# Optimization experiments

Measured on AMD Instinct MI355X. Metric: run time of the kernel, lower is better.

Reference implementation:

```python
import jax, jax.numpy as jnp
import numpy as np

IN_F, HID, OUT_F = 171, 1024, 171

def _cond_lst(condition_num, groundtruth_num, seq_len):
    num_cycles = seq_len // (condition_num + groundtruth_num) + 1
    lst = np.zeros((num_cycles, condition_num + groundtruth_num), dtype=np.float32)
    lst[:, :groundtruth_num] = 1.0
    return lst.reshape(-1)[:seq_len]

def setup_inputs() -> dict:
    key = jax.random.key(0)
    ks = jax.random.split(key, 16)
    s = 0.02
    inp = {
        'real_seq': jax.random.normal(ks[0], (128, 128, IN_F), jnp.float32),
        'W_ih1': jax.random.normal(ks[1], (4 * HID, IN_F), jnp.float32) * s,
        'W_hh1': jax.random.normal(ks[2], (4 * HID, HID), jnp.float32) * s,
        'b_ih1': jnp.zeros((4 * HID,), jnp.float32),
        'b_hh1': jnp.zeros((4 * HID,), jnp.float32),
        'W_ih2': jax.random.normal(ks[3], (4 * HID, HID), jnp.float32) * s,
        'W_hh2': jax.random.normal(ks[4], (4 * HID, HID), jnp.float32) * s,
        'b_ih2': jnp.zeros((4 * HID,), jnp.float32),
        'b_hh2': jnp.zeros((4 * HID,), jnp.float32),
        'W_ih3': jax.random.normal(ks[5], (4 * HID, HID), jnp.float32) * s,
        'W_hh3': jax.random.normal(ks[6], (4 * HID, HID), jnp.float32) * s,
        'b_ih3': jnp.zeros((4 * HID,), jnp.float32),
        'b_hh3': jnp.zeros((4 * HID,), jnp.float32),
        'W_dec': jax.random.normal(ks[7], (OUT_F, HID), jnp.float32) * s,
        'b_dec': jnp.zeros((OUT_F,), jnp.float32),
        'condition_num': 5,
        'groundtruth_num': 5,
    }
    return inp

def _lstm_cell(x, h, c, Wih, Whh, bih, bhh):
    # PyTorch LSTMCell: gates ordered i, f, g, o
    g = x @ Wih.T + bih + h @ Whh.T + bhh
    i, f, gg, o = jnp.split(g, 4, axis=-1)
    c2 = jax.nn.sigmoid(f) * c + jax.nn.sigmoid(i) * jnp.tanh(gg)
    h2 = jax.nn.sigmoid(o) * jnp.tanh(c2)
    return h2, c2

def reference(real_seq, W_ih1, W_hh1, b_ih1, b_hh1, W_ih2, W_hh2, b_ih2, b_hh2,
              W_ih3, W_hh3, b_ih3, b_hh3, W_dec, b_dec, condition_num, groundtruth_num):
    B, T, _ = real_seq.shape
    cond = jnp.asarray(_cond_lst(condition_num, groundtruth_num, T))  # [T], 1=use ground truth
    z = jnp.zeros((B, HID), jnp.float32)
    carry0 = (z, z, z, z, z, z, jnp.zeros((B, OUT_F), jnp.float32))
    xs = (jnp.swapaxes(real_seq, 0, 1), cond)  # time-major

    def step(carry, x):
        h0, h1, h2, c0, c1, c2, out_frame = carry
        frame, c_flag = x
        in_frame = jnp.where(c_flag > 0.5, frame, out_frame)
        h0, c0 = _lstm_cell(in_frame, h0, c0, W_ih1, W_hh1, b_ih1, b_hh1)
        h1, c1 = _lstm_cell(h0, h1, c1, W_ih2, W_hh2, b_ih2, b_hh2)
        h2, c2 = _lstm_cell(h1, h2, c2, W_ih3, W_hh3, b_ih3, b_hh3)
        out_frame = h2 @ W_dec.T + b_dec
        return (h0, h1, h2, c0, c1, c2, out_frame), out_frame

    _, out_seq = jax.lax.scan(step, carry0, xs)  # [T, B, OUT_F]
    return jnp.swapaxes(out_seq, 0, 1)  # [B, T, OUT_F]
```

## Files before the change

kernel.cpp:

```cpp
#include <hip/hip_runtime.h>

#define TT 128
#define INF 171

typedef _Float16 half8 __attribute__((ext_vector_type(8)));
typedef float floatx4 __attribute__((ext_vector_type(4)));
typedef unsigned short u16;

#define XBSZ 163840
#define HSZ  131072

__device__ __forceinline__ u16 f2h(float f){
  _Float16 h = (_Float16)f;
  return __builtin_bit_cast(u16, h);
}
__device__ __forceinline__ float sigm(float x){ return 1.f/(1.f+__expf(-x)); }
__device__ __forceinline__ float tanh_(float x){ return 1.f - 2.f/(__expf(2.f*x)+1.f); }

__device__ __forceinline__ void scat_coh(u16* buf, int nch, int b, int k, u16 v){
  u16* p = buf + (size_t)((((b>>4)*nch + (k>>5))*4 + ((k>>3)&3))*16 + (b&15))*8 + (k&7);
  unsigned int vv = v;
  asm volatile("global_store_short %0, %1, off sc0 sc1" :: "v"(p), "v"(vv) : "memory");
}
__device__ __forceinline__ void ld16_coh(half8& d, const u16* p){
  asm volatile("global_load_dwordx4 %0, %1, off sc0 sc1" : "=&v"(d) : "v"(p) : "memory");
}

__global__ __launch_bounds__(256) void prep_w1f(const float* __restrict__ Wih1,
    const float* __restrict__ Whh1, u16* __restrict__ Wf){
  int u = blockIdx.x*256 + threadIdx.x;
  int tile = u / 2560;
  int r = u - tile*2560;
  int kc = r >> 6, l = r & 63;
  int row = (tile>>6)*1024 + (tile&63)*16 + (l&15);
  int k0 = kc*32 + ((l>>4)<<3);
  half8 hv;
  #pragma unroll
  for (int e=0;e<8;e++){
    int k = k0+e;
    float w = 0.f;
    if (k < 171)       w = Wih1[(size_t)row*171 + k];
    else if (k < 1195) w = Whh1[(size_t)row*1024 + (k-171)];
    hv[e] = (_Float16)w;
  }
  *(half8*)&Wf[(size_t)(tile*40 + kc)*512 + (size_t)l*8] = hv;
}

__global__ __launch_bounds__(256) void prep_w23f(const float* __restrict__ Wih2,
    const float* __restrict__ Whh2, const float* __restrict__ Wih3,
    const float* __restrict__ Whh3, u16* __restrict__ W2f, u16* __restrict__ W3f){
  int u = blockIdx.x*256 + threadIdx.x;
  int tile = u >> 12;
  int r = u & 4095;
  int kc = r >> 6, l = r & 63;
  int row = (tile>>6)*1024 + (tile&63)*16 + (l&15);
  int k0 = kc*32 + ((l>>4)<<3);
  half8 h2, h3;
  #pragma unroll
  for (int e=0;e<8;e++){
    int k = k0+e;
    size_t si = (size_t)row*1024 + (k & 1023);
    h2[e] = (_Float16)((k < 1024) ? Wih2[si] : Whh2[si]);
    h3[e] = (_Float16)((k < 1024) ? Wih3[si] : Whh3[si]);
  }
  size_t base = (size_t)(tile*64 + kc)*512 + (size_t)l*8;
  *(half8*)&W2f[base] = h2;
  *(half8*)&W3f[base] = h3;
}

__global__ __launch_bounds__(256) void prep_wdecf(const float* __restrict__ Wdec,
    u16* __restrict__ Wdf){
  int u = blockIdx.x*256 + threadIdx.x;
  int tile = u / 2048;
  int r = u & 2047;
  int kc = r >> 6, l = r & 63;
  int row = tile*16 + (l&15);
  int k0 = kc*32 + ((l>>4)<<3);
  half8 hv;
  #pragma unroll
  for (int e=0;e<8;e++){
    int k = k0+e;
    hv[e] = (_Float16)((row < 171) ? Wdec[(size_t)row*1024 + k] : 0.f);
  }
  *(half8*)&Wdf[(size_t)(tile*32 + kc)*512 + (size_t)l*8] = hv;
}

__global__ __launch_bounds__(256) void prep_misc(
    const float* __restrict__ rseq, const int* __restrict__ gnp,
    const float* __restrict__ bih1, const float* __restrict__ bhh1,
    const float* __restrict__ bih2, const float* __restrict__ bhh2,
    const float* __restrict__ bih3, const float* __restrict__ bhh3,
    const float* __restrict__ bdec,
    u16* __restrict__ Xb1f, u16* __restrict__ Hf, float* __restrict__ cbuf,
    float* __restrict__ b1, float* __restrict__ b2, float* __restrict__ b3,
    float* __restrict__ bd, int* __restrict__ bar)
{
  size_t idx = (size_t)blockIdx.x*256 + threadIdx.x;
  if (idx < 327680){
    int q = (int)(idx / 163840);
    int rem = (int)(idx % 163840);
    int btile = rem / 20480;
    int r2 = rem % 20480;
    int kc = r2 >> 9, r3 = r2 & 511;
    int l = r3 >> 3, e = r3 & 7;
    int b = btile*16 + (l&15);
    int k = kc*32 + ((l>>4)<<3) + e;
    float v = 0.f;
    if (q==0 && k < 171 && *gnp > 0) v = rseq[(size_t)b*TT*INF + k];
    Xb1f[idx] = f2h(v);
    return;
  }
  idx -= 327680;
  if (idx < 786432){ Hf[idx] = 0; return; }
  idx -= 786432;
  if (idx < 393216){ cbuf[idx] = 0.f; return; }
  idx -= 393216;
  if (idx < 12288){
    int which = (int)(idx >> 12), j = (int)(idx & 4095);
    float v = (which==0)? (bih1[j]+bhh1[j]) : (which==1)? (bih2[j]+bhh2[j]) : (bih3[j]+bhh3[j]);
    ((which==0)?b1:(which==1)?b2:b3)[j] = v;
    return;
  }
  idx -= 12288;
  if (idx < 176){ bd[idx] = (idx < 171) ? bdec[idx] : 0.f; return; }
  idx -= 176;
  if (idx < 512) bar[idx] = 0;
}

__device__ __forceinline__ void gridbar(int* __restrict__ bar, int bId, int bc, int* s_dead){
  asm volatile("s_waitcnt vmcnt(0)" ::: "memory");
  __syncthreads();
  if (threadIdx.x == 0 && !(*s_dead)){
    int* c1  = &bar[(bId & 7) * 32];
    int* c0  = &bar[288];
    int* gen = &bar[320];
    bool released = false;
    int o1 = __hip_atomic_fetch_add(c1, 1, __ATOMIC_RELAXED, __HIP_MEMORY_SCOPE_AGENT);
    if ((o1 & 31) == 31){
      int o0 = __hip_atomic_fetch_add(c0, 1, __ATOMIC_RELAXED, __HIP_MEMORY_SCOPE_AGENT);
      if ((o0 & 7) == 7){
        __hip_atomic_fetch_add(gen, 1, __ATOMIC_RELAXED, __HIP_MEMORY_SCOPE_AGENT);
        released = true;
      }
    }
    if (!released){
      long long t0 = clock64();
      while (__hip_atomic_fetch_add(gen, 0, __ATOMIC_RELAXED, __HIP_MEMORY_SCOPE_AGENT) < bc + 1){
        __builtin_amdgcn_s_sleep(8);
        if (clock64() - t0 > 30000000LL){ *s_dead = 1; break; }
      }
    }
  }
  __syncthreads();
}

template<int NC, int NBC>
__device__ __forceinline__ void stage(const u16* const* srcs, u16* XL, int tid){
  half8 v[NC*NBC];
  #pragma unroll
  for (int c=0;c<NC;c++){
    #pragma unroll
    for (int i=0;i<NBC;i++)
      ld16_coh(v[c*NBC+i], srcs[c] + (size_t)i*4096 + (size_t)tid*8);
  }
  asm volatile("s_waitcnt vmcnt(0)" ::: "memory");
  __builtin_amdgcn_sched_barrier(0);
  #pragma unroll
  for (int c=0;c<NC;c++){
    #pragma unroll
    for (int i=0;i<NBC;i++)
      *(half8*)&XL[(size_t)(c*NBC+i)*4096 + (size_t)tid*8] = v[c*NBC+i];
  }
}

template<int KHALF, int GS, bool NT>
__device__ __forceinline__ void gemm_lds(const u16* __restrict__ wp,
    const u16* __restrict__ x0, const u16* __restrict__ x1,
    floatx4& a0, floatx4& a1)
{
  constexpr int NG = KHALF/GS;
  half8 W[2][GS];
  #pragma unroll
  for (int i=0;i<GS;i++)
    W[0][i] = NT ? __builtin_nontemporal_load((const half8*)(wp + (size_t)i*512))
                 : *(const half8*)(wp + (size_t)i*512);
  #pragma unroll
  for (int g8=0; g8<NG; g8++){
    const int cur = g8 & 1, nxt = cur ^ 1;
    if (g8+1 < NG){
      const size_t off = (size_t)(g8+1)*GS*512;
      #pragma unroll
      for (int i=0;i<GS;i++)
        W[nxt][i] = NT ? __builtin_nontemporal_load((const half8*)(wp + off + (size_t)i*512))
                       : *(const half8*)(wp + off + (size_t)i*512);
    }
    #pragma unroll
    for (int i=0;i<GS;i++){
      half8 xv0 = *(const half8*)(x0 + (size_t)(g8*GS+i)*512);
      half8 xv1 = *(const half8*)(x1 + (size_t)(g8*GS+i)*512);
      a0 = __builtin_amdgcn_mfma_f32_16x16x32_f16(W[cur][i], xv0, a0, 0,0,0);
      a1 = __builtin_amdgcn_mfma_f32_16x16x32_f16(W[cur][i], xv1, a1, 0,0,0);
    }
  }
}

template<bool NT>
__device__ __forceinline__ void layer23(
    const u16* __restrict__ Wl, const float* __restrict__ bb, float* __restrict__ cb,
    const u16* __restrict__ xa, const u16* __restrict__ xh, u16* __restrict__ hd,
    u16* XL, float (*gb)[16][33],
    int js, int nq, int tid, int w, int l, int g, int hf, int l15, int lq)
{
  const u16* srcs[4] = {
    xa + (size_t)(nq*2  )*16384, xa + (size_t)(nq*2+1)*16384,
    xh + (size_t)(nq*2  )*16384, xh + (size_t)(nq*2+1)*16384 };
  stage<4,4>(srcs, XL, tid);
  __syncthreads();
  const u16* wp = Wl + ((size_t)(g*64 + js)*64 + (size_t)hf*32)*512 + (size_t)(l<<3);
  const u16* x0 = XL + (size_t)hf*32768 + (size_t)(l<<3);
  const u16* x1 = x0 + 16384;
  floatx4 a0{}, a1{};
  gemm_lds<32,8,NT>(wp, x0, x1, a0, a1);
  #pragma unroll
  for (int r=0;r<4;r++){
    gb[w][lq*4+r][l15]      = a0[r];
    gb[w][lq*4+r][16 + l15] = a1[r];
  }
  __syncthreads();
  {
    int uu = tid >> 5, bq = tid & 31;
    int j = js*16 + uu, bg = nq*32 + bq;
    float gi = gb[0][uu][bq] + gb[1][uu][bq] + bb[j];
    float gf = gb[2][uu][bq] + gb[3][uu][bq] + bb[1024 + j];
    float gg = gb[4][uu][bq] + gb[5][uu][bq] + bb[2048 + j];
    float go = gb[6][uu][bq] + gb[7][uu][bq] + bb[3072 + j];
    size_t ci = (size_t)j*128 + bg;
    float c = sigm(gf)*cb[ci] + sigm(gi)*tanh_(gg);
    cb[ci] = c;
    u16 hb = f2h(sigm(go)*tanh_(c));
    scat_coh(hd, 32, bg, j, hb);
  }
}

__global__ void __launch_bounds__(512,2) acro_persist(
    const u16* __restrict__ W1f, const u16* __restrict__ W2f,
    const u16* __restrict__ W3f, const u16* __restrict__ Wdf,
    u16* __restrict__ Xb1f, u16* __restrict__ Hf, float* __restrict__ cbuf,
    const float* __restrict__ b1, const float* __restrict__ b2,
    const float* __restrict__ b3, const float* __restrict__ bd,
    const float* __restrict__ rseq, float* __restrict__ out,
    const int* __restrict__ cnp, const int* __restrict__ gnp, int* __restrict__ bar)
{
  __shared__ u16 XL[65536];
  __shared__ float gb[8][16][33];
  __shared__ int s_dead;
  const int bId = (int)blockIdx.x;
  const int js = (bId & 7)*8 + ((bId >> 5) & 7);
  const int nq = (bId >> 3) & 3;
  const int tid = (int)threadIdx.x;
  const int w = tid >> 6, l = tid & 63;
  const int g = w >> 1, hf = w & 1;
  const int l15 = l & 15, lq = l >> 4;
  if (tid == 0) s_dead = 0;
  const int gnv = *gnp;
  int P = *cnp + gnv; if (P < 1) P = 1;
  int bc = 0;

  u16* H0[2] = { Hf,          Hf + HSZ   };
  u16* H1[2] = { Hf + 2*HSZ,  Hf + 3*HSZ };
  u16* H2[2] = { Hf + 4*HSZ,  Hf + 5*HSZ };

  __syncthreads();
  for (int t=0; t<TT; t++){
    const int pr = t & 1, nx = pr ^ 1;

    {
      const u16* xb = Xb1f + (size_t)pr*XBSZ;
      const u16* srcs[2] = { xb + (size_t)(nq*2)*20480, xb + (size_t)(nq*2+1)*20480 };
      stage<2,5>(srcs, XL, tid);
      __syncthreads();
      const u16* wp = W1f + ((size_t)(g*64 + js)*40 + (size_t)hf*20)*512 + (size_t)(l<<3);
      const u16* x0 = XL + (size_t)hf*10240 + (size_t)(l<<3);
      const u16* x1 = x0 + 20480;
      floatx4 a0{}, a1{};
      gemm_lds<20,4,false>(wp, x0, x1, a0, a1);
      #pragma unroll
      for (int r=0;r<4;r++){
        gb[w][lq*4+r][l15]      = a0[r];
        gb[w][lq*4+r][16 + l15] = a1[r];
      }
      __syncthreads();
      {
        int uu = tid >> 5, bq = tid & 31;
        int j = js*16 + uu, bg = nq*32 + bq;
        float gi = gb[0][uu][bq] + gb[1][uu][bq] + b1[j];
        float gf = gb[2][uu][bq] + gb[3][uu][bq] + b1[1024 + j];
        float gg = gb[4][uu][bq] + gb[5][uu][bq] + b1[2048 + j];
        float go = gb[6][uu][bq] + gb[7][uu][bq] + b1[3072 + j];
        size_t ci = (size_t)j*128 + bg;
        float c = sigm(gf)*cbuf[ci] + sigm(gi)*tanh_(gg);
        cbuf[ci] = c;
        u16 hb = f2h(sigm(go)*tanh_(c));
        scat_coh(H0[pr], 32, bg, j, hb);
        scat_coh(Xb1f + (size_t)nx*XBSZ, 40, bg, 171 + j, hb);
      }
    }
    gridbar(bar, bId, bc, &s_dead); bc++;

    layer23<false>(W2f, b2, cbuf + 131072, H0[pr], H1[nx], H1[pr],
                   XL, gb, js, nq, tid, w, l, g, hf, l15, lq);
    gridbar(bar, bId, bc, &s_dead); bc++;
    layer23<true >(W3f, b3, cbuf + 262144, H1[pr], H2[nx], H2[pr],
                   XL, gb, js, nq, tid, w, l, g, hf, l15, lq);
    gridbar(bar, bId, bc, &s_dead); bc++;

    if (bId < 44){
      const int tile = bId >> 2, dq = bId & 3;
      const u16* srcs[2] = { H2[pr] + (size_t)(dq*2)*16384, H2[pr] + (size_t)(dq*2+1)*16384 };
      stage<2,4>(srcs, XL, tid);
      __syncthreads();
      const u16* wp = Wdf + (size_t)(tile*32 + w*4)*512 + (size_t)(l<<3);
      const u16* x0 = XL + (size_t)(w*4)*512 + (size_t)(l<<3);
      const u16* x1 = x0 + 16384;
      floatx4 d0{}, d1{};
      #pragma unroll
      for (int i=0;i<4;i++){
        half8 wv  = *(const half8*)(wp + (size_t)i*512);
        half8 a0v = *(const half8*)(x0 + (size_t)i*512);
        half8 a1v = *(const half8*)(x1 + (size_t)i*512);
        d0 = __builtin_amdgcn_mfma_f32_16x16x32_f16(wv, a0v, d0, 0,0,0);
        d1 = __builtin_amdgcn_mfma_f32_16x16x32_f16(wv, a1v, d1, 0,0,0);
      }
      #pragma unroll
      for (int r=0;r<4;r++){
        gb[w][lq*4+r][l15]      = d0[r];
        gb[w][lq*4+r][16 + l15] = d1[r];
      }
      __syncthreads();
      const int nf = (((t+1) % P) < gnv) ? 1 : 0;
      {
        int uu = tid >> 5, bq = tid & 31;
        int o = tile*16 + uu, b = dq*32 + bq;
        if (o < 171){
          float v = bd[o];
          #pragma unroll
          for (int i=0;i<8;i++) v += gb[i][uu][bq];
          out[((size_t)b*TT + t)*INF + o] = v;
          if (t+1 < TT){
            float src = nf ? rseq[((size_t)b*TT + (t+1))*INF + o] : v;
            scat_coh(Xb1f + (size_t)nx*XBSZ, 40, b, o, f2h(src));
          }
        }
      }
    }
    gridbar(bar, bId, bc, &s_dead); bc++;
  }
}

extern "C" void kernel_launch(void* const* d_in, const int* in_sizes, int n_in,
                              void* d_out, int out_size, void* d_ws, size_t ws_size,
                              hipStream_t stream)
{
  const float* rseq = (const float*)d_in[0];
  const float* Wih1 = (const float*)d_in[1];
  const float* Whh1 = (const float*)d_in[2];
  const float* bih1 = (const float*)d_in[3];
  const float* bhh1 = (const float*)d_in[4];
  const float* Wih2 = (const float*)d_in[5];
  const float* Whh2 = (const float*)d_in[6];
  const float* bih2 = (const float*)d_in[7];
  const float* bhh2 = (const float*)d_in[8];
  const float* Wih3 = (const float*)d_in[9];
  const float* Whh3 = (const float*)d_in[10];
  const float* bih3 = (const float*)d_in[11];
  const float* bhh3 = (const float*)d_in[12];
  const float* Wdec = (const float*)d_in[13];
  const float* bdec = (const float*)d_in[14];
  const int* cn = (const int*)d_in[15];
  const int* gn = (const int*)d_in[16];
  float* out = (float*)d_out;

  char* p = (char*)d_ws;
  auto take = [&](size_t n){ void* r = (void*)p; p += (n + 255) & ~(size_t)255; return r; };
  u16* W1f  = (u16*)take(5242880UL*2);
  u16* W2f  = (u16*)take(8388608UL*2);
  u16* W3f  = (u16*)take(8388608UL*2);
  u16* Wdf  = (u16*)take(180224UL*2);
  u16* Xb1f = (u16*)take(327680UL*2);
  u16* Hf   = (u16*)take(786432UL*2);
  float* cbuf = (float*)take(393216UL*4);
  float* b1 = (float*)take(4096*4);
  float* b2 = (float*)take(4096*4);
  float* b3 = (float*)take(4096*4);
  float* bd = (float*)take(176*4);
  int* bar  = (int*)take(512*4);
  if ((size_t)(p - (char*)d_ws) > ws_size) return;

  prep_w1f  <<<2560,256,0,stream>>>(Wih1, Whh1, W1f);
  prep_w23f <<<4096,256,0,stream>>>(Wih2, Whh2, Wih3, Whh3, W2f, W3f);
  prep_wdecf<<<88,  256,0,stream>>>(Wdec, Wdf);
  prep_misc <<<5939,256,0,stream>>>(rseq, gn, bih1,bhh1,bih2,bhh2,bih3,bhh3,bdec,
                                    Xb1f, Hf, cbuf, b1,b2,b3,bd, bar);

  acro_persist<<<256,512,0,stream>>>(W1f, W2f, W3f, Wdf, Xb1f, Hf, cbuf,
                                     b1, b2, b3, bd, rseq, out, cn, gn, bar);
}
```

Before: 4.944 ms.

## Keep layer-1/2 and decoder weights, biases and cell state in registers

Each block now loads its slices of the layer-1, layer-2 and decoder weights into registers once before the time loop. Biases and the three LSTM cell states are also held in registers instead of being reread from or written to global memory every step. Layer 3 still streams its weights from memory, now without nontemporal loads, and the grid-barrier spin sleep is shortened. The register footprint grows a lot (about 56 half8 vectors per thread at 512 threads with launch_bounds 2), which risks spills or reduced occupancy that could break the persistent co-residency the grid barrier relies on.

```diff
diff --git a/kernel.cpp b/kernel.cpp
--- a/kernel.cpp
+++ b/kernel.cpp
@@ -146,7 +146,7 @@
     if (!released){
       long long t0 = clock64();
       while (__hip_atomic_fetch_add(gen, 0, __ATOMIC_RELAXED, __HIP_MEMORY_SCOPE_AGENT) < bc + 1){
-        __builtin_amdgcn_s_sleep(8);
+        __builtin_amdgcn_s_sleep(2);
         if (clock64() - t0 > 30000000LL){ *s_dead = 1; break; }
       }
     }
@@ -173,8 +173,8 @@
   }
 }
 
-template<int KHALF, int GS, bool NT>
-__device__ __forceinline__ void gemm_lds(const u16* __restrict__ wp,
+template<int KHALF, int GS>
+__device__ __forceinline__ void gemm_stream(const u16* __restrict__ wp,
     const u16* __restrict__ x0, const u16* __restrict__ x1,
     floatx4& a0, floatx4& a1)
 {
@@ -182,8 +182,7 @@
   half8 W[2][GS];
   #pragma unroll
   for (int i=0;i<GS;i++)
-    W[0][i] = NT ? __builtin_nontemporal_load((const half8*)(wp + (size_t)i*512))
-                 : *(const half8*)(wp + (size_t)i*512);
+    W[0][i] = *(const half8*)(wp + (size_t)i*512);
   #pragma unroll
   for (int g8=0; g8<NG; g8++){
     const int cur = g8 & 1, nxt = cur ^ 1;
@@ -191,8 +190,7 @@
       const size_t off = (size_t)(g8+1)*GS*512;
       #pragma unroll
       for (int i=0;i<GS;i++)
-        W[nxt][i] = NT ? __builtin_nontemporal_load((const half8*)(wp + off + (size_t)i*512))
-                       : *(const half8*)(wp + off + (size_t)i*512);
+        W[nxt][i] = *(const half8*)(wp + off + (size_t)i*512);
     }
     #pragma unroll
     for (int i=0;i<GS;i++){
@@ -204,48 +202,10 @@
   }
 }
 
-template<bool NT>
-__device__ __forceinline__ void layer23(
-    const u16* __restrict__ Wl, const float* __restrict__ bb, float* __restrict__ cb,
-    const u16* __restrict__ xa, const u16* __restrict__ xh, u16* __restrict__ hd,
-    u16* XL, float (*gb)[16][33],
-    int js, int nq, int tid, int w, int l, int g, int hf, int l15, int lq)
-{
-  const u16* srcs[4] = {
-    xa + (size_t)(nq*2  )*16384, xa + (size_t)(nq*2+1)*16384,
-    xh + (size_t)(nq*2  )*16384, xh + (size_t)(nq*2+1)*16384 };
-  stage<4,4>(srcs, XL, tid);
-  __syncthreads();
-  const u16* wp = Wl + ((size_t)(g*64 + js)*64 + (size_t)hf*32)*512 + (size_t)(l<<3);
-  const u16* x0 = XL + (size_t)hf*32768 + (size_t)(l<<3);
-  const u16* x1 = x0 + 16384;
-  floatx4 a0{}, a1{};
-  gemm_lds<32,8,NT>(wp, x0, x1, a0, a1);
-  #pragma unroll
-  for (int r=0;r<4;r++){
-    gb[w][lq*4+r][l15]      = a0[r];
-    gb[w][lq*4+r][16 + l15] = a1[r];
-  }
-  __syncthreads();
-  {
-    int uu = tid >> 5, bq = tid & 31;
-    int j = js*16 + uu, bg = nq*32 + bq;
-    float gi = gb[0][uu][bq] + gb[1][uu][bq] + bb[j];
-    float gf = gb[2][uu][bq] + gb[3][uu][bq] + bb[1024 + j];
-    float gg = gb[4][uu][bq] + gb[5][uu][bq] + bb[2048 + j];
-    float go = gb[6][uu][bq] + gb[7][uu][bq] + bb[3072 + j];
-    size_t ci = (size_t)j*128 + bg;
-    float c = sigm(gf)*cb[ci] + sigm(gi)*tanh_(gg);
-    cb[ci] = c;
-    u16 hb = f2h(sigm(go)*tanh_(c));
-    scat_coh(hd, 32, bg, j, hb);
-  }
-}
-
 __global__ void __launch_bounds__(512,2) acro_persist(
     const u16* __restrict__ W1f, const u16* __restrict__ W2f,
     const u16* __restrict__ W3f, const u16* __restrict__ Wdf,
-    u16* __restrict__ Xb1f, u16* __restrict__ Hf, float* __restrict__ cbuf,
+    u16* __restrict__ Xb1f, u16* __restrict__ Hf,
     const float* __restrict__ b1, const float* __restrict__ b2,
     const float* __restrict__ b3, const float* __restrict__ bd,
     const float* __restrict__ rseq, float* __restrict__ out,
@@ -261,6 +221,8 @@
   const int w = tid >> 6, l = tid & 63;
   const int g = w >> 1, hf = w & 1;
   const int l15 = l & 15, lq = l >> 4;
+  const int uu = tid >> 5, bq = tid & 31;
+  const int jj = js*16 + uu, bgg = nq*32 + bq;
   if (tid == 0) s_dead = 0;
   const int gnv = *gnp;
   int P = *cnp + gnv; if (P < 1) P = 1;
@@ -270,6 +232,37 @@
   u16* H1[2] = { Hf + 2*HSZ,  Hf + 3*HSZ };
   u16* H2[2] = { Hf + 4*HSZ,  Hf + 5*HSZ };
 
+  half8 W1r[20], W2r[32], Wdr[4];
+  {
+    const u16* wp = W1f + ((size_t)(g*64 + js)*40 + (size_t)hf*20)*512 + (size_t)(l<<3);
+    #pragma unroll
+    for (int i=0;i<20;i++) W1r[i] = *(const half8*)(wp + (size_t)i*512);
+  }
+  {
+    const u16* wp = W2f + ((size_t)(g*64 + js)*64 + (size_t)hf*32)*512 + (size_t)(l<<3);
+    #pragma unroll
+    for (int i=0;i<32;i++) W2r[i] = *(const half8*)(wp + (size_t)i*512);
+  }
+  const int dtile = bId >> 2, dq_ = bId & 3;
+  const int oo = dtile*16 + uu;
+  if (bId < 44){
+    const u16* wp = Wdf + (size_t)(dtile*32 + w*4)*512 + (size_t)(l<<3);
+    #pragma unroll
+    for (int i=0;i<4;i++) Wdr[i] = *(const half8*)(wp + (size_t)i*512);
+  } else {
+    #pragma unroll
+    for (int i=0;i<4;i++) Wdr[i] = half8{};
+  }
+  float bs1[4], bs2[4], bs3[4];
+  #pragma unroll
+  for (int q=0;q<4;q++){
+    bs1[q] = b1[q*1024 + jj];
+    bs2[q] = b2[q*1024 + jj];
+    bs3[q] = b3[q*1024 + jj];
+  }
+  const float bdr = (bId < 44) ? bd[oo] : 0.f;
+  float c0r = 0.f, c1r = 0.f, c2r = 0.f;
+
   __syncthreads();
   for (int t=0; t<TT; t++){
     const int pr = t & 1, nx = pr ^ 1;
@@ -279,11 +272,16 @@
       const u16* srcs[2] = { xb + (size_t)(nq*2)*20480, xb + (size_t)(nq*2+1)*20480 };
       stage<2,5>(srcs, XL, tid);
       __syncthreads();
-      const u16* wp = W1f + ((size_t)(g*64 + js)*40 + (size_t)hf*20)*512 + (size_t)(l<<3);
       const u16* x0 = XL + (size_t)hf*10240 + (size_t)(l<<3);
       const u16* x1 = x0 + 20480;
       floatx4 a0{}, a1{};
-      gemm_lds<20,4,false>(wp, x0, x1, a0, a1);
+      #pragma unroll
+      for (int i=0;i<20;i++){
+        half8 xv0 = *(const half8*)(x0 + (size_t)i*512);
+        half8 xv1 = *(const half8*)(x1 + (size_t)i*512);
+        a0 = __builtin_amdgcn_mfma_f32_16x16x32_f16(W1r[i], xv0, a0, 0,0,0);
+        a1 = __builtin_amdgcn_mfma_f32_16x16x32_f16(W1r[i], xv1, a1, 0,0,0);
+      }
       #pragma unroll
       for (int r=0;r<4;r++){
         gb[w][lq*4+r][l15]      = a0[r];
@@ -291,45 +289,101 @@
       }
       __syncthreads();
       {
-        int uu = tid >> 5, bq = tid & 31;
-        int j = js*16 + uu, bg = nq*32 + bq;
-        float gi = gb[0][uu][bq] + gb[1][uu][bq] + b1[j];
-        float gf = gb[2][uu][bq] + gb[3][uu][bq] + b1[1024 + j];
-        float gg = gb[4][uu][bq] + gb[5][uu][bq] + b1[2048 + j];
-        float go = gb[6][uu][bq] + gb[7][uu][bq] + b1[3072 + j];
-        size_t ci = (size_t)j*128 + bg;
-        float c = sigm(gf)*cbuf[ci] + sigm(gi)*tanh_(gg);
-        cbuf[ci] = c;
+        float gi = gb[0][uu][bq] + gb[1][uu][bq] + bs1[0];
+        float gf = gb[2][uu][bq] + gb[3][uu][bq] + bs1[1];
+        float gg = gb[4][uu][bq] + gb[5][uu][bq] + bs1[2];
+        float go = gb[6][uu][bq] + gb[7][uu][bq] + bs1[3];
+        float c = sigm(gf)*c0r + sigm(gi)*tanh_(gg);
+        c0r = c;
         u16 hb = f2h(sigm(go)*tanh_(c));
-        scat_coh(H0[pr], 32, bg, j, hb);
-        scat_coh(Xb1f + (size_t)nx*XBSZ, 40, bg, 171 + j, hb);
+        scat_coh(H0[pr], 32, bgg, jj, hb);
+        scat_coh(Xb1f + (size_t)nx*XBSZ, 40, bgg, 171 + jj, hb);
       }
     }
     gridbar(bar, bId, bc, &s_dead); bc++;
 
-    layer23<false>(W2f, b2, cbuf + 131072, H0[pr], H1[nx], H1[pr],
-                   XL, gb, js, nq, tid, w, l, g, hf, l15, lq);
+    {
+      const u16* xa = H0[pr];
+      const u16* xh = H1[nx];
+      const u16* srcs[4] = {
+        xa + (size_t)(nq*2  )*16384, xa + (size_t)(nq*2+1)*16384,
+        xh + (size_t)(nq*2  )*16384, xh + (size_t)(nq*2+1)*16384 };
+      stage<4,4>(srcs, XL, tid);
+      __syncthreads();
+      const u16* x0 = XL + (size_t)hf*32768 + (size_t)(l<<3);
+      const u16* x1 = x0 + 16384;
+      floatx4 a0{}, a1{};
+      #pragma unroll
+      for (int i=0;i<32;i++){
+        half8 xv0 = *(const half8*)(x0 + (size_t)i*512);
+        half8 xv1 = *(const half8*)(x1 + (size_t)i*512);
+        a0 = __builtin_amdgcn_mfma_f32_16x16x32_f16(W2r[i], xv0, a0, 0,0,0);
+        a1 = __builtin_amdgcn_mfma_f32_16x16x32_f16(W2r[i], xv1, a1, 0,0,0);
+      }
+      #pragma unroll
+      for (int r=0;r<4;r++){
+        gb[w][lq*4+r][l15]      = a0[r];
+        gb[w][lq*4+r][16 + l15] = a1[r];
+      }
+      __syncthreads();
+      {
+        float gi = gb[0][uu][bq] + gb[1][uu][bq] + bs2[0];
+        float gf = gb[2][uu][bq] + gb[3][uu][bq] + bs2[1];
+        float gg = gb[4][uu][bq] + gb[5][uu][bq] + bs2[2];
+        float go = gb[6][uu][bq] + gb[7][uu][bq] + bs2[3];
+        float c = sigm(gf)*c1r + sigm(gi)*tanh_(gg);
+        c1r = c;
+        u16 hb = f2h(sigm(go)*tanh_(c));
+        scat_coh(H1[pr], 32, bgg, jj, hb);
+      }
+    }
     gridbar(bar, bId, bc, &s_dead); bc++;
-    layer23<true >(W3f, b3, cbuf + 262144, H1[pr], H2[nx], H2[pr],
-                   XL, gb, js, nq, tid, w, l, g, hf, l15, lq);
+
+    {
+      const u16* xa = H1[pr];
+      const u16* xh = H2[nx];
+      const u16* srcs[4] = {
+        xa + (size_t)(nq*2  )*16384, xa + (size_t)(nq*2+1)*16384,
+        xh + (size_t)(nq*2  )*16384, xh + (size_t)(nq*2+1)*16384 };
+      stage<4,4>(srcs, XL, tid);
+      __syncthreads();
+      const u16* wp = W3f + ((size_t)(g*64 + js)*64 + (size_t)hf*32)*512 + (size_t)(l<<3);
+      const u16* x0 = XL + (size_t)hf*32768 + (size_t)(l<<3);
+      const u16* x1 = x0 + 16384;
+      floatx4 a0{}, a1{};
+      gemm_stream<32,8>(wp, x0, x1, a0, a1);
+      #pragma unroll
+      for (int r=0;r<4;r++){
+        gb[w][lq*4+r][l15]      = a0[r];
+        gb[w][lq*4+r][16 + l15] = a1[r];
+      }
+      __syncthreads();
+      {
+        float gi = gb[0][uu][bq] + gb[1][uu][bq] + bs3[0];
+        float gf = gb[2][uu][bq] + gb[3][uu][bq] + bs3[1];
+        float gg = gb[4][uu][bq] + gb[5][uu][bq] + bs3[2];
+        float go = gb[6][uu][bq] + gb[7][uu][bq] + bs3[3];
+        float c = sigm(gf)*c2r + sigm(gi)*tanh_(gg);
+        c2r = c;
+        u16 hb = f2h(sigm(go)*tanh_(c));
+        scat_coh(H2[pr], 32, bgg, jj, hb);
+      }
+    }
     gridbar(bar, bId, bc, &s_dead); bc++;
 
     if (bId < 44){
-      const int tile = bId >> 2, dq = bId & 3;
-      const u16* srcs[2] = { H2[pr] + (size_t)(dq*2)*16384, H2[pr] + (size_t)(dq*2+1)*16384 };
+      const u16* srcs[2] = { H2[pr] + (size_t)(dq_*2)*16384, H2[pr] + (size_t)(dq_*2+1)*16384 };
       stage<2,4>(srcs, XL, tid);
       __syncthreads();
-      const u16* wp = Wdf + (size_t)(tile*32 + w*4)*512 + (size_t)(l<<3);
       const u16* x0 = XL + (size_t)(w*4)*512 + (size_t)(l<<3);
       const u16* x1 = x0 + 16384;
       floatx4 d0{}, d1{};
       #pragma unroll
       for (int i=0;i<4;i++){
-        half8 wv  = *(const half8*)(wp + (size_t)i*512);
         half8 a0v = *(const half8*)(x0 + (size_t)i*512);
         half8 a1v = *(const half8*)(x1 + (size_t)i*512);
-        d0 = __builtin_amdgcn_mfma_f32_16x16x32_f16(wv, a0v, d0, 0,0,0);
-        d1 = __builtin_amdgcn_mfma_f32_16x16x32_f16(wv, a1v, d1, 0,0,0);
+        d0 = __builtin_amdgcn_mfma_f32_16x16x32_f16(Wdr[i], a0v, d0, 0,0,0);
+        d1 = __builtin_amdgcn_mfma_f32_16x16x32_f16(Wdr[i], a1v, d1, 0,0,0);
       }
       #pragma unroll
       for (int r=0;r<4;r++){
@@ -338,18 +392,15 @@
       }
       __syncthreads();
       const int nf = (((t+1) % P) < gnv) ? 1 : 0;
-      {
-        int uu = tid >> 5, bq = tid & 31;
-        int o = tile*16 + uu, b = dq*32 + bq;
-        if (o < 171){
-          float v = bd[o];
-          #pragma unroll
-          for (int i=0;i<8;i++) v += gb[i][uu][bq];
-          out[((size_t)b*TT + t)*INF + o] = v;
-          if (t+1 < TT){
-            float src = nf ? rseq[((size_t)b*TT + (t+1))*INF + o] : v;
-            scat_coh(Xb1f + (size_t)nx*XBSZ, 40, b, o, f2h(src));
-          }
+      if (oo < 171){
+        float v = bdr;
+        #pragma unroll
+        for (int i=0;i<8;i++) v += gb[i][uu][bq];
+        int b = dq_*32 + bq;
+        out[((size_t)b*TT + t)*INF + oo] = v;
+        if (t+1 < TT){
+          float src = nf ? rseq[((size_t)b*TT + (t+1))*INF + oo] : v;
+          scat_coh(Xb1f + (size_t)nx*XBSZ, 40, b, oo, f2h(src));
         }
       }
     }
@@ -402,6 +453,6 @@
   prep_misc <<<5939,256,0,stream>>>(rseq, gn, bih1,bhh1,bih2,bhh2,bih3,bhh3,bdec,
                                     Xb1f, Hf, cbuf, b1,b2,b3,bd, bar);
 
-  acro_persist<<<256,512,0,stream>>>(W1f, W2f, W3f, Wdf, Xb1f, Hf, cbuf,
+  acro_persist<<<256,512,0,stream>>>(W1f, W2f, W3f, Wdf, Xb1f, Hf,
                                      b1, b2, b3, bd, rseq, out, cn, gn, bar);
 }
```

Result: slower. 5.052 ms (+2.2%).
